# Performance work log

Hardware: AMD Instinct MI355X
Metric: run time of the kernel (lower is better)

## Reference

```python
import jax, jax.numpy as jnp
import numpy as np

BS, HW, HIDDEN, TOK, NTOK = 32, 1024, 256, 768, 2048


def setup_inputs() -> dict:
    key = jax.random.key(0)
    ks = jax.random.split(key, 6)
    s = 0.02  # init scale for weights
    return {
        "src": jax.random.normal(ks[0], (HW, BS, HIDDEN), jnp.float32),
        "codebook": jax.random.normal(ks[1], (NTOK, TOK), jnp.float32),
        "w_head": jax.random.normal(ks[2], (TOK, HIDDEN), jnp.float32) * s,
        "w_tail": jax.random.normal(ks[3], (HIDDEN, TOK), jnp.float32) * s,
        "w_pos": jax.random.normal(ks[4], (TOK, TOK), jnp.float32) * s,
        "b_pos": jnp.zeros((TOK,), jnp.float32),
        "w_gate": jax.random.normal(ks[5], (2, 2 * TOK), jnp.float32) * s,
        "h": 32,
        "w": 32,
    }


def reference(src, codebook, w_head, w_tail, w_pos, b_pos, w_gate, h, w):
    N, bs, hidden = src.shape  # [num_visu_token, bs, hidden_dim]
    tok = codebook.shape[1]
    # permute(1,2,0).view(bs,-1,h,w)
    x = jnp.transpose(src, (1, 2, 0)).reshape(bs, hidden, h, w)
    # conv_head: 1x1 conv, no bias
    xq = jnp.einsum("bchw,oc->bohw", x, w_head)  # [bs, tok, h, w]
    # raw-memory reshape, matches torch .view(-1, token_dim)
    flat = xq.reshape(-1, tok)  # [bs*h*w, tok]
    d = (
        jnp.sum(flat * flat, axis=1, keepdims=True)
        - 2.0 * flat @ codebook.T
        + jnp.sum(codebook * codebook, axis=1)[None, :]
    )
    indices = jnp.argmin(d, axis=1)  # [bs*h*w]
    quantized = codebook[indices]  # gather
    # straight-through estimator
    quantized = flat + jax.lax.stop_gradient(quantized - flat)
    # pos_align linear
    quantized = quantized @ w_pos.T + b_pos
    # view(bs, N, tok).permute(0,2,1).view(bs,-1,h,w)
    emb = jnp.transpose(quantized.reshape(bs, N, tok), (0, 2, 1)).reshape(bs, tok, h, w)
    # gated fusion
    gate_in = jnp.concatenate([emb, xq], axis=1)  # [bs, 2*tok, h, w]
    scores = jax.nn.softmax(jnp.einsum("bchw,oc->bohw", gate_in, w_gate), axis=1)
    fused = emb * scores[:, 0:1] + xq * scores[:, 1:2]
    # conv_tail 1x1, then flatten(2).permute(2,0,1)
    out = jnp.einsum("bchw,oc->bohw", fused, w_tail)  # [bs, hidden, h, w]
    out = jnp.transpose(out.reshape(bs, hidden, -1), (2, 0, 1))  # [h*w, bs, hidden]
    return out, indices
```

## Files before the change

### kernel.cpp

```cpp
#include <hip/hip_runtime.h>
#include <cstdint>

#define BSZ 32
#define NVIS 1024
#define HID 256
#define TOKD 768
#define NCODE 2048
#define NPIX 32768

typedef unsigned short u16;
typedef _Float16 half8 __attribute__((ext_vector_type(8)));
typedef unsigned short ushort8 __attribute__((ext_vector_type(8)));
using f32x4 = __attribute__((ext_vector_type(4))) float;

#define AS1 __attribute__((address_space(1)))
#define AS3 __attribute__((address_space(3)))

__device__ __forceinline__ f32x4 mfmaF16(half8 a, half8 b, f32x4 c) {
  return __builtin_amdgcn_mfma_f32_16x16x32_f16(a, b, c, 0, 0, 0);
}

__device__ __forceinline__ unsigned long long pack_key(float d, int idx) {
  unsigned int b = __float_as_uint(d);
  b = (b & 0x80000000u) ? ~b : (b | 0x80000000u);
  return ((unsigned long long)b << 32) | (unsigned int)idx;
}

__device__ __forceinline__ void split16(float v, u16& h, u16& l) {
  union { _Float16 f; u16 u; } a, b;
  a.f = (_Float16)v;
  float hf = (float)a.f;
  b.f = (_Float16)(v - hf);
  h = a.u; l = b.u;
}

__global__ __launch_bounds__(256)
void prep1(const float* __restrict__ cb, const float* __restrict__ wh,
           const float* __restrict__ wt, const float* __restrict__ wp,
           const float* __restrict__ wg, const float* __restrict__ bp,
           u16* __restrict__ cbh, u16* __restrict__ cbl,
           u16* __restrict__ whh, u16* __restrict__ whl,
           float* __restrict__ cbn, float* __restrict__ Mm, float* __restrict__ uv,
           float* __restrict__ Gt, float* __restrict__ g2,
           float* __restrict__ ct0, float* __restrict__ cg) {
  const int bid = blockIdx.x, tid = threadIdx.x;
  if (bid < 6144) {
    int i = bid*256 + tid;
    u16 h, l; split16(cb[i], h, l);
    cbh[i] = h; cbl[i] = l;
  } else if (bid < 6912) {
    int i = (bid - 6144)*256 + tid;
    u16 h, l; split16(wh[i], h, l);
    whh[i] = h; whl[i] = l;
  } else if (bid < 7424) {
    int n = (bid - 6912)*4 + (tid >> 6);
    int lane = tid & 63;
    float a = 0.f;
#pragma unroll
    for (int i = 0; i < 12; ++i) { float v = cb[(long)n*TOKD + lane + 64*i]; a += v*v; }
#pragma unroll
    for (int off = 32; off; off >>= 1) a += __shfl_down(a, off);
    if (lane == 0) cbn[n] = a;
  } else if (bid < 7680) {
    int c2 = bid - 7424, c1 = tid;
    float acc = 0.f;
    for (int t = 0; t < TOKD; ++t) acc += wh[t*HID + c1] * wt[(long)c2*TOKD + t];
    Mm[c1*HID + c2] = acc;
  } else if (bid < 7682) {
    int o = bid - 7680, c1 = tid;
    float acc = 0.f;
    for (int t = 0; t < TOKD; ++t) acc += wh[t*HID + c1] * wg[o*(2*TOKD) + TOKD + t];
    uv[o*HID + c1] = acc;
  } else if (bid < 8450) {
    int rbid = bid - 7682;
    int c = rbid & 255, part = rbid >> 8;
    int tp = part*256 + tid;
    float acc = 0.f;
    for (int t = 0; t < TOKD; ++t) acc += wt[(long)c*TOKD + t] * wp[(long)t*TOKD + tp];
    Gt[(long)tp*HID + c] = acc;
  } else if (bid < 8453) {
    int tp = (bid - 8450)*256 + tid;
    float a0 = 0.f, a1 = 0.f;
    for (int t = 0; t < TOKD; ++t) {
      float wv = wp[(long)t*TOKD + tp];
      a0 += wv * wg[t];
      a1 += wv * wg[2*TOKD + t];
    }
    g2[tp] = a0; g2[TOKD + tp] = a1;
  } else if (bid < 8454) {
    int c = tid;
    float a = 0.f;
    for (int t = 0; t < TOKD; ++t) a += bp[t] * wt[(long)c*TOKD + t];
    ct0[c] = a;
  } else {
    int o = tid >> 6, lane = tid & 63;
    if (o < 2) {
      float a = 0.f;
      for (int t = lane; t < TOKD; t += 64) a += bp[t] * wg[o*(2*TOKD) + t];
#pragma unroll
      for (int off = 32; off; off >>= 1) a += __shfl_down(a, off);
      if (lane == 0) cg[o] = a;
    }
  }
}

__global__ __launch_bounds__(256)
void prep2(const float* __restrict__ cb, const float* __restrict__ Gt,
           const float* __restrict__ ct0, const float* __restrict__ g2,
           const float* __restrict__ cg, float* __restrict__ tc,
           float* __restrict__ gA) {
  __shared__ float cbs[8][TOKD];
  const int n0 = blockIdx.x * 8, tid = threadIdx.x;
  for (int i = tid; i < 8*TOKD; i += 256) cbs[i / TOKD][i % TOKD] = cb[(long)n0*TOKD + i];
  __syncthreads();
  float acc[8] = {};
  for (int t = 0; t < TOKD; ++t) {
    float gv = Gt[(long)t*HID + tid];
#pragma unroll
    for (int i = 0; i < 8; ++i) acc[i] += cbs[i][t] * gv;
  }
  float c0v = ct0[tid];
#pragma unroll
  for (int i = 0; i < 8; ++i) tc[(long)(n0+i)*HID + tid] = acc[i] + c0v;
  {
    int i = tid >> 5, l32 = tid & 31;
    float a0 = 0.f, a1 = 0.f;
    for (int t = l32; t < TOKD; t += 32) {
      float cv = cbs[i][t];
      a0 += cv * g2[t];
      a1 += cv * g2[TOKD + t];
    }
#pragma unroll
    for (int off = 16; off; off >>= 1) { a0 += __shfl_down(a0, off); a1 += __shfl_down(a1, off); }
    if (l32 == 0) { gA[n0+i] = a0 + cg[0]; gA[NCODE + n0+i] = a1 + cg[1]; }
  }
}

__global__ __launch_bounds__(256)
void head_mfma(const u16* __restrict__ whh, const u16* __restrict__ whl,
               const float* __restrict__ src,
               u16* __restrict__ xqh, u16* __restrict__ xql) {
  __shared__ u16 SM[32768] __attribute__((aligned(16)));
  u16* Ah = SM;
  u16* Al = SM + 8192;
  u16* Bh = SM + 16384;
  u16* Bl = SM + 24576;
  const int tid = threadIdx.x, lane = tid & 63, w = tid >> 6;
  const int n = lane & 15, q = lane >> 4;
  const int rh = w & 1, ch = w >> 1;
  const int obase = blockIdx.x * 128, pbase = blockIdx.y * 128, b = blockIdx.z;

  auto stageA = [&](int kc, int buf) {
#pragma unroll
    for (int is = 0; is < 2; ++is) {
      int c = is*256 + tid;
      int t = c >> 6, qq = (c >> 4) & 3, nn = c & 15;
      long off = (long)(obase + t*16 + nn)*HID + kc*32 + qq*8;
      __builtin_amdgcn_global_load_lds((AS1 void*)(whh + off),
          (AS3 void*)&Ah[buf*4096 + c*8], 16, 0, 0);
      __builtin_amdgcn_global_load_lds((AS1 void*)(whl + off),
          (AS3 void*)&Al[buf*4096 + c*8], 16, 0, 0);
    }
  };
  auto stageB = [&](int kc, int buf) {
#pragma unroll
    for (int is = 0; is < 2; ++is) {
      int c = is*256 + tid;
      int t = c >> 6, qq = (c >> 4) & 3, nn = c & 15;
      const float* gp = src + ((long)(pbase + t*16 + nn)*BSZ + b)*HID + kc*32 + qq*8;
      float4 v0 = *(const float4*)gp;
      float4 v1 = *(const float4*)(gp + 4);
      float vv[8] = {v0.x, v0.y, v0.z, v0.w, v1.x, v1.y, v1.z, v1.w};
      ushort8 hv, lv;
#pragma unroll
      for (int j = 0; j < 8; ++j) { u16 hs, ls; split16(vv[j], hs, ls); hv[j] = hs; lv[j] = ls; }
      *(ushort8*)&Bh[buf*4096 + c*8] = hv;
      *(ushort8*)&Bl[buf*4096 + c*8] = lv;
    }
  };

  f32x4 acc[4][4];
#pragma unroll
  for (int i = 0; i < 4; ++i)
#pragma unroll
    for (int j = 0; j < 4; ++j) acc[i][j] = (f32x4){0.f, 0.f, 0.f, 0.f};

  stageA(0, 0); stageB(0, 0);
  __syncthreads();

  for (int kt = 0; kt < HID/32; ++kt) {
    const int buf = kt & 1;
    if (kt + 1 < HID/32) { stageA(kt + 1, buf ^ 1); stageB(kt + 1, buf ^ 1); }
    half8 af[4][2], bf[4][2];
#pragma unroll
    for (int rt = 0; rt < 4; ++rt) {
      int idx = buf*4096 + ((rh*4 + rt)*64 + q*16 + n)*8;
      af[rt][0] = *(const half8*)&Ah[idx];
      af[rt][1] = *(const half8*)&Al[idx];
    }
#pragma unroll
    for (int ct = 0; ct < 4; ++ct) {
      int idx = buf*4096 + ((ch*4 + ct)*64 + q*16 + n)*8;
      bf[ct][0] = *(const half8*)&Bh[idx];
      bf[ct][1] = *(const half8*)&Bl[idx];
    }
#pragma unroll
    for (int rt = 0; rt < 4; ++rt)
#pragma unroll
      for (int ct = 0; ct < 4; ++ct) {
        acc[rt][ct] = mfmaF16(af[rt][0], bf[ct][0], acc[rt][ct]);
        acc[rt][ct] = mfmaF16(af[rt][0], bf[ct][1], acc[rt][ct]);
        acc[rt][ct] = mfmaF16(af[rt][1], bf[ct][0], acc[rt][ct]);
      }
    __syncthreads();
  }

#pragma unroll
  for (int pass = 0; pass < 2; ++pass) {
    u16* dst = pass ? xql : xqh;
#pragma unroll
    for (int rt = 0; rt < 4; ++rt)
#pragma unroll
      for (int ct = 0; ct < 4; ++ct)
#pragma unroll
        for (int reg = 0; reg < 4; ++reg) {
          u16 hs, ls; split16(acc[rt][ct][reg], hs, ls);
          int ol = rh*64 + rt*16 + q*4 + reg;
          int pl = ch*64 + ct*16 + n;
          SM[ol*136 + pl] = pass ? ls : hs;
        }
    __syncthreads();
#pragma unroll
    for (int s = 0; s < 8; ++s) {
      int cc = tid*8 + s;
      int o = cc >> 4, p8 = cc & 15;
      ushort8 v = *(const ushort8*)&SM[o*136 + p8*8];
      *(ushort8*)(dst + ((long)b*TOKD + obase + o)*NVIS + pbase + p8*8) = v;
    }
    __syncthreads();
  }
}

__global__ __launch_bounds__(256)
void retile(u16* __restrict__ bufH, u16* __restrict__ bufL) {
  __shared__ u16 T[96*136] __attribute__((aligned(16)));
  const long tile = blockIdx.x;
  const int tid = threadIdx.x;
#pragma unroll
  for (int pass = 0; pass < 2; ++pass) {
    u16* buf = pass ? bufL : bufH;
    if (pass) __syncthreads();
#pragma unroll
    for (int i = 0; i < 6; ++i) {
      int g = i*256 + tid;
      int row = g / 96, c16 = g % 96;
      ushort8 v = *(const ushort8*)(buf + tile*12288 + row*768 + c16*8);
      *(ushort8*)&T[c16*136 + row*8] = v;
    }
    __syncthreads();
#pragma unroll
    for (int i = 0; i < 6; ++i) {
      int g = i*256 + tid;
      int kc = g >> 6, lp = g & 63;
      int q = lp >> 4, n = lp & 15;
      ushort8 v = *(const ushort8*)&T[(kc*4 + q)*136 + n*8];
      *(ushort8*)(buf + tile*12288 + (long)kc*512 + lp*8) = v;
    }
  }
}

#define LOADK(kc_, Ar, Br)                                              \
  {                                                                     \
    const int kcv = (kc_);                                              \
    const int seg = (kcv >= 48) ? 2 : ((kcv >= 24) ? 1 : 0);            \
    const int kk = kcv - seg*24;                                        \
    const u16* pa = ((seg == 1) ? pal : pah) + kk*512;                  \
    const u16* pb = ((seg == 2) ? pbl : pbh) + kk*512;                  \
    _Pragma("unroll")                                                   \
    for (int i = 0; i < 4; ++i) {                                       \
      Ar[i] = *(const half8*)(pa + (long)i*12288);                      \
      Br[i] = *(const half8*)(pb + (long)i*12288);                      \
    }                                                                   \
  }

#define MFMASET(Ar, Br)                                                 \
  {                                                                     \
    _Pragma("unroll")                                                   \
    for (int rt = 0; rt < 4; ++rt)                                      \
      _Pragma("unroll")                                                 \
      for (int ct = 0; ct < 4; ++ct)                                    \
        acc[rt][ct] = mfmaF16(Ar[rt], Br[ct], acc[rt][ct]);             \
  }

__global__ __launch_bounds__(256, 2)
void vq_mfma(const u16* __restrict__ xqh, const u16* __restrict__ xql,
             const u16* __restrict__ cbh, const u16* __restrict__ cbl,
             const float* __restrict__ cbn, unsigned long long* __restrict__ keys) {
  const int bid = blockIdx.x;
  const int rb = bid >> 4, cblk = bid & 15;
  const int tid = threadIdx.x, lane = tid & 63, w = tid >> 6;
  const int n = lane & 15, q = lane >> 4;
  const int wr = w & 1, wc = w >> 1;
  const int rT0 = rb*8 + wr*4;
  const int cT0 = cblk*8 + wc*4;

  const u16* pah = xqh + (long)rT0*12288 + lane*8;
  const u16* pal = xql + (long)rT0*12288 + lane*8;
  const u16* pbh = cbh + (long)cT0*12288 + lane*8;
  const u16* pbl = cbl + (long)cT0*12288 + lane*8;

  f32x4 acc[4][4];
#pragma unroll
  for (int a = 0; a < 4; ++a)
#pragma unroll
    for (int b2 = 0; b2 < 4; ++b2) acc[a][b2] = (f32x4){0.f, 0.f, 0.f, 0.f};

  half8 A0[4], A1[4], A2[4], A3[4];
  half8 B0[4], B1[4], B2[4], B3[4];

  LOADK(0, A0, B0);
  LOADK(1, A1, B1);
  LOADK(2, A2, B2);

  for (int kc2 = 0; kc2 < 18; ++kc2) {
    const int kc = kc2 * 4;
    if (kc + 3 < 72) LOADK(kc + 3, A3, B3);
    MFMASET(A0, B0);
    if (kc + 4 < 72) LOADK(kc + 4, A0, B0);
    MFMASET(A1, B1);
    if (kc + 5 < 72) LOADK(kc + 5, A1, B1);
    MFMASET(A2, B2);
    if (kc + 6 < 72) LOADK(kc + 6, A2, B2);
    MFMASET(A3, B3);
  }

  float cbv[4];
#pragma unroll
  for (int ct = 0; ct < 4; ++ct) cbv[ct] = cbn[(cT0 + ct)*16 + n];
#pragma unroll
  for (int rt = 0; rt < 4; ++rt) {
#pragma unroll
    for (int reg = 0; reg < 4; ++reg) {
      float bd = 3.4e38f; int bi = 0;
#pragma unroll
      for (int ct = 0; ct < 4; ++ct) {
        float d = cbv[ct] - 2.0f * acc[rt][ct][reg];
        int code = (cT0 + ct)*16 + n;
        if (d < bd) { bd = d; bi = code; }
      }
      unsigned long long k = pack_key(bd, bi);
      unsigned long long v;
      v = __shfl_xor(k, 1); k = (v < k) ? v : k;
      v = __shfl_xor(k, 2); k = (v < k) ? v : k;
      v = __shfl_xor(k, 4); k = (v < k) ? v : k;
      v = __shfl_xor(k, 8); k = (v < k) ? v : k;
      if (n == 0) {
        int row = (rT0 + rt)*16 + q*4 + reg;
        atomicMin(&keys[row], k);
      }
    }
  }
}

__global__ __launch_bounds__(256)
void fuse_out(const float* __restrict__ src, const unsigned long long* __restrict__ keys,
              const float* __restrict__ gA, const float* __restrict__ uvec,
              const float* __restrict__ Mm, const float* __restrict__ tailcode,
              float* __restrict__ out, float* __restrict__ outIdx) {
  __shared__ float ss[32][257];
  __shared__ float s0s[32];
  __shared__ int ids[32];
  const int tid = threadIdx.x;
  const int rb = blockIdx.x * 32;
  const int b = rb >> 10;
  const int p0 = rb & 1023;
#pragma unroll
  for (int qq = 0; qq < 32; ++qq)
    ss[qq][tid] = src[(long)(p0 + qq) * (BSZ*HID) + b*HID + tid];
  if (tid < 32) {
    unsigned long long u = keys[rb + tid];
    int id = (int)(unsigned int)(u & 0xFFFFFFFFull);
    ids[tid] = id;
    outIdx[rb + tid] = (float)id;
  }
  __syncthreads();
  {
    const int wv = tid >> 6, lane = tid & 63;
    for (int qq = 0; qq < 8; ++qq) {
      int qp = wv*8 + qq;
      float a0 = 0.f, a1 = 0.f;
#pragma unroll
      for (int i = 0; i < 4; ++i) {
        float v = ss[qp][lane + 64*i];
        a0 += v * uvec[lane + 64*i];
        a1 += v * uvec[HID + lane + 64*i];
      }
#pragma unroll
      for (int off = 32; off; off >>= 1) { a0 += __shfl_down(a0, off); a1 += __shfl_down(a1, off); }
      if (lane == 0) {
        int id = ids[qp];
        float l0 = gA[id] + a0;
        float l1 = gA[NCODE + id] + a1;
        s0s[qp] = 1.0f / (1.0f + expf(l1 - l0));
      }
    }
  }
  __syncthreads();
  const int qg = tid >> 5, cg = tid & 31;
  const int q0 = qg * 4, c0 = cg * 8;
  float acc[4][8] = {};
  for (int cp = 0; cp < HID; ++cp) {
    float4 m0 = *(const float4*)(Mm + cp*HID + c0);
    float4 m1 = *(const float4*)(Mm + cp*HID + c0 + 4);
    float mm[8] = {m0.x,m0.y,m0.z,m0.w,m1.x,m1.y,m1.z,m1.w};
#pragma unroll
    for (int i = 0; i < 4; ++i) {
      float sv = ss[q0+i][cp];
#pragma unroll
      for (int j = 0; j < 8; ++j) acc[i][j] += sv * mm[j];
    }
  }
#pragma unroll
  for (int i = 0; i < 4; ++i) {
    int qp = q0 + i;
    int id = ids[qp];
    float s0 = s0s[qp], s1 = 1.0f - s0;
    const float* tc = tailcode + (long)id*HID + c0;
    float* op = out + (long)(p0+qp)*(BSZ*HID) + b*HID + c0;
    float4 o0, o1;
    o0.x = s0*tc[0] + s1*acc[i][0]; o0.y = s0*tc[1] + s1*acc[i][1];
    o0.z = s0*tc[2] + s1*acc[i][2]; o0.w = s0*tc[3] + s1*acc[i][3];
    o1.x = s0*tc[4] + s1*acc[i][4]; o1.y = s0*tc[5] + s1*acc[i][5];
    o1.z = s0*tc[6] + s1*acc[i][6]; o1.w = s0*tc[7] + s1*acc[i][7];
    *(float4*)(op) = o0; *(float4*)(op+4) = o1;
  }
}

extern "C" void kernel_launch(void* const* d_in, const int* in_sizes, int n_in,
                              void* d_out, int out_size, void* d_ws, size_t ws_size,
                              hipStream_t stream) {
  const float* src    = (const float*)d_in[0];
  const float* cb     = (const float*)d_in[1];
  const float* w_head = (const float*)d_in[2];
  const float* w_tail = (const float*)d_in[3];
  const float* w_pos  = (const float*)d_in[4];
  const float* b_pos  = (const float*)d_in[5];
  const float* w_gate = (const float*)d_in[6];
  float* out = (float*)d_out;

  char* wsp = (char*)d_ws;
  size_t off = 0;
  auto alloc = [&](size_t bytes) {
    off = (off + 255) & ~(size_t)255;
    void* p = wsp + off; off += bytes; return p;
  };
  u16* xqh = (u16*)alloc((size_t)BSZ*TOKD*NVIS*2);
  u16* xql = (u16*)alloc((size_t)BSZ*TOKD*NVIS*2);
  u16* cbh = (u16*)alloc((size_t)NCODE*TOKD*2);
  u16* cbl = (u16*)alloc((size_t)NCODE*TOKD*2);
  u16* whh = (u16*)alloc((size_t)TOKD*HID*2);
  u16* whl = (u16*)alloc((size_t)TOKD*HID*2);
  float* cbn      = (float*)alloc((size_t)NCODE*4);
  float* Gt       = (float*)alloc((size_t)TOKD*HID*4);
  float* g2       = (float*)alloc((size_t)2*TOKD*4);
  float* ct0      = (float*)alloc((size_t)HID*4);
  float* cg       = (float*)alloc((size_t)2*4);
  float* tailcode = (float*)alloc((size_t)NCODE*HID*4);
  float* gA       = (float*)alloc((size_t)2*NCODE*4);
  float* Mm       = (float*)alloc((size_t)HID*HID*4);
  float* uvec     = (float*)alloc((size_t)2*HID*4);
  unsigned long long* keys = (unsigned long long*)alloc((size_t)NPIX*8);
  (void)ws_size; (void)in_sizes; (void)n_in; (void)out_size;

  prep1<<<8455, 256, 0, stream>>>(cb, w_head, w_tail, w_pos, w_gate, b_pos,
                                  cbh, cbl, whh, whl, cbn, Mm, uvec, Gt, g2, ct0, cg);
  retile<<<NCODE/16, 256, 0, stream>>>(cbh, cbl);
  prep2<<<NCODE/8, 256, 0, stream>>>(cb, Gt, ct0, g2, cg, tailcode, gA);

  head_mfma<<<dim3(TOKD/128, NVIS/128, BSZ), 256, 0, stream>>>(whh, whl, src, xqh, xql);
  retile<<<NPIX/16, 256, 0, stream>>>(xqh, xql);

  hipMemsetAsync(keys, 0xFF, (size_t)NPIX*8, stream);
  vq_mfma<<<4096, 256, 0, stream>>>(xqh, xql, cbh, cbl, cbn, keys);

  fuse_out<<<NPIX/32, 256, 0, stream>>>(src, keys, gA, uvec, Mm, tailcode,
                                        out, out + (size_t)NVIS*BSZ*HID);
}
```

Before: 747.7 us.

## Stage VQ distance GEMM tiles through LDS with async global-to-LDS loads

Rewrites the VQ distance kernel so each 512-thread block computes a 256x256 tile. Operands go through a 4-deep LDS ring filled with global_load_lds, in place of each wave loading its own fragments straight from global memory into registers. Each wave now keeps an 8x4 accumulator grid and reads A/B fragments from shared memory, so global traffic per MFMA drops through block-level reuse. The cost is two barriers per k-step, larger register use (32 accumulators) that may hurt occupancy, and reliance on hand-written vmcnt waits being correct.

```diff
diff --git a/kernel.cpp b/kernel.cpp
--- a/kernel.cpp
+++ b/kernel.cpp
@@ -269,83 +269,79 @@
   }
 }
 
-#define LOADK(kc_, Ar, Br)                                              \
-  {                                                                     \
-    const int kcv = (kc_);                                              \
-    const int seg = (kcv >= 48) ? 2 : ((kcv >= 24) ? 1 : 0);            \
-    const int kk = kcv - seg*24;                                        \
-    const u16* pa = ((seg == 1) ? pal : pah) + kk*512;                  \
-    const u16* pb = ((seg == 2) ? pbl : pbh) + kk*512;                  \
-    _Pragma("unroll")                                                   \
-    for (int i = 0; i < 4; ++i) {                                       \
-      Ar[i] = *(const half8*)(pa + (long)i*12288);                      \
-      Br[i] = *(const half8*)(pb + (long)i*12288);                      \
-    }                                                                   \
-  }
-
-#define MFMASET(Ar, Br)                                                 \
-  {                                                                     \
-    _Pragma("unroll")                                                   \
-    for (int rt = 0; rt < 4; ++rt)                                      \
-      _Pragma("unroll")                                                 \
-      for (int ct = 0; ct < 4; ++ct)                                    \
-        acc[rt][ct] = mfmaF16(Ar[rt], Br[ct], acc[rt][ct]);             \
-  }
-
-__global__ __launch_bounds__(256, 2)
+__global__ __launch_bounds__(512, 2)
 void vq_mfma(const u16* __restrict__ xqh, const u16* __restrict__ xql,
              const u16* __restrict__ cbh, const u16* __restrict__ cbl,
              const float* __restrict__ cbn, unsigned long long* __restrict__ keys) {
+  __shared__ u16 SM[65536] __attribute__((aligned(16)));
   const int bid = blockIdx.x;
-  const int rb = bid >> 4, cblk = bid & 15;
+  const int rowBlk = bid >> 3, codeBlk = bid & 7;
+  const int rowTile0 = rowBlk * 16, codeTile0 = codeBlk * 16;
   const int tid = threadIdx.x, lane = tid & 63, w = tid >> 6;
   const int n = lane & 15, q = lane >> 4;
-  const int wr = w & 1, wc = w >> 1;
-  const int rT0 = rb*8 + wr*4;
-  const int cT0 = cblk*8 + wc*4;
-
-  const u16* pah = xqh + (long)rT0*12288 + lane*8;
-  const u16* pal = xql + (long)rT0*12288 + lane*8;
-  const u16* pbh = cbh + (long)cT0*12288 + lane*8;
-  const u16* pbl = cbl + (long)cT0*12288 + lane*8;
-
-  f32x4 acc[4][4];
-#pragma unroll
-  for (int a = 0; a < 4; ++a)
+  const int wr = w >> 2, wc = w & 3;
+
+  const size_t aOff = (size_t)(rowTile0 + 2*w) * 12288 + lane*8;
+  const size_t bOff = (size_t)(codeTile0 + 2*w) * 12288 + lane*8;
+  const int ldsChunk = (2*w)*512 + lane*8;
+
+  auto STAGE = [&](int ht, int buf) {
+    const int seg = (ht >= 48) ? 2 : ((ht >= 24) ? 1 : 0);
+    const int kk = ht - seg * 24;
+    const u16* pa = ((seg == 1) ? xql : xqh) + aOff + kk*512;
+    const u16* pb = ((seg == 2) ? cbl : cbh) + bOff + kk*512;
+    u16* la = &SM[buf*8192 + ldsChunk];
+    u16* lb = &SM[32768 + buf*8192 + ldsChunk];
+    __builtin_amdgcn_global_load_lds((AS1 void*)pa,           (AS3 void*)la,        16, 0, 0);
+    __builtin_amdgcn_global_load_lds((AS1 void*)(pa + 12288), (AS3 void*)(la + 512), 16, 0, 0);
+    __builtin_amdgcn_global_load_lds((AS1 void*)pb,           (AS3 void*)lb,        16, 0, 0);
+    __builtin_amdgcn_global_load_lds((AS1 void*)(pb + 12288), (AS3 void*)(lb + 512), 16, 0, 0);
+  };
+
+  f32x4 acc[8][4];
+#pragma unroll
+  for (int a = 0; a < 8; ++a)
 #pragma unroll
     for (int b2 = 0; b2 < 4; ++b2) acc[a][b2] = (f32x4){0.f, 0.f, 0.f, 0.f};
 
-  half8 A0[4], A1[4], A2[4], A3[4];
-  half8 B0[4], B1[4], B2[4], B3[4];
-
-  LOADK(0, A0, B0);
-  LOADK(1, A1, B1);
-  LOADK(2, A2, B2);
-
-  for (int kc2 = 0; kc2 < 18; ++kc2) {
-    const int kc = kc2 * 4;
-    if (kc + 3 < 72) LOADK(kc + 3, A3, B3);
-    MFMASET(A0, B0);
-    if (kc + 4 < 72) LOADK(kc + 4, A0, B0);
-    MFMASET(A1, B1);
-    if (kc + 5 < 72) LOADK(kc + 5, A1, B1);
-    MFMASET(A2, B2);
-    if (kc + 6 < 72) LOADK(kc + 6, A2, B2);
-    MFMASET(A3, B3);
+  STAGE(0, 0); STAGE(1, 1); STAGE(2, 2);
+
+#pragma unroll 4
+  for (int ht = 0; ht < 72; ++ht) {
+    const int pf = (ht + 3 > 71) ? 71 : ht + 3;
+    STAGE(pf, (ht + 3) & 3);
+    asm volatile("s_waitcnt vmcnt(12)" ::: "memory");
+    asm volatile("s_barrier" ::: "memory");
+    const int abase = (ht & 3)*8192 + (wr*8)*512 + lane*8;
+    const int bbase = 32768 + (ht & 3)*8192 + (wc*4)*512 + lane*8;
+    half8 Af[8], Bf[4];
+#pragma unroll
+    for (int rt = 0; rt < 8; ++rt) Af[rt] = *(const half8*)&SM[abase + rt*512];
+#pragma unroll
+    for (int ct = 0; ct < 4; ++ct) Bf[ct] = *(const half8*)&SM[bbase + ct*512];
+    asm volatile("s_waitcnt lgkmcnt(0)" ::: "memory");
+    asm volatile("s_barrier" ::: "memory");
+    __builtin_amdgcn_s_setprio(1);
+#pragma unroll
+    for (int rt = 0; rt < 8; ++rt)
+#pragma unroll
+      for (int ct = 0; ct < 4; ++ct)
+        acc[rt][ct] = mfmaF16(Af[rt], Bf[ct], acc[rt][ct]);
+    __builtin_amdgcn_s_setprio(0);
   }
 
   float cbv[4];
 #pragma unroll
-  for (int ct = 0; ct < 4; ++ct) cbv[ct] = cbn[(cT0 + ct)*16 + n];
-#pragma unroll
-  for (int rt = 0; rt < 4; ++rt) {
+  for (int ct = 0; ct < 4; ++ct) cbv[ct] = cbn[(codeTile0 + wc*4 + ct)*16 + n];
+#pragma unroll
+  for (int rt = 0; rt < 8; ++rt) {
 #pragma unroll
     for (int reg = 0; reg < 4; ++reg) {
       float bd = 3.4e38f; int bi = 0;
 #pragma unroll
       for (int ct = 0; ct < 4; ++ct) {
         float d = cbv[ct] - 2.0f * acc[rt][ct][reg];
-        int code = (cT0 + ct)*16 + n;
+        int code = (codeTile0 + wc*4 + ct)*16 + n;
         if (d < bd) { bd = d; bi = code; }
       }
       unsigned long long k = pack_key(bd, bi);
@@ -355,7 +351,7 @@
       v = __shfl_xor(k, 4); k = (v < k) ? v : k;
       v = __shfl_xor(k, 8); k = (v < k) ? v : k;
       if (n == 0) {
-        int row = (rT0 + rt)*16 + q*4 + reg;
+        int row = (rowTile0 + wr*8 + rt)*16 + q*4 + reg;
         atomicMin(&keys[row], k);
       }
     }
@@ -481,7 +477,7 @@
   retile<<<NPIX/16, 256, 0, stream>>>(xqh, xql);
 
   hipMemsetAsync(keys, 0xFF, (size_t)NPIX*8, stream);
-  vq_mfma<<<4096, 256, 0, stream>>>(xqh, xql, cbh, cbl, cbn, keys);
+  vq_mfma<<<1024, 512, 0, stream>>>(xqh, xql, cbh, cbl, cbn, keys);
 
   fuse_out<<<NPIX/32, 256, 0, stream>>>(src, keys, gA, uvec, Mm, tailcode,
                                         out, out + (size_t)NVIS*BSZ*HID);
```

Result: faster. 667.2 us (-10.8%).
